# Performance work log

Hardware: AMD Instinct MI355X
Metric: run time of the kernel (lower is better)

## Reference

```python
import jax, jax.numpy as jnp
import numpy as np

B, T, D = 2, 2048, 1024   # batch, seq, d_model
E, K, H = 8, 2, 704       # routed experts, topk, expert hidden
SH = 704 * 2              # shared-expert hidden = moe_hidden * num_shared_experts
EPS = 1e-20               # topk_norm_epsilon
STD = 0.02                # init_weight_std


def setup_inputs() -> dict:
    key = jax.random.key(0)
    ks = jax.random.split(key, 8)
    return {
        "x":   jax.random.normal(ks[0], (B, T, D), jnp.float32),
        "Wg":  jax.random.normal(ks[1], (E, D), jnp.float32) * STD,   # router experts_weights
        "W1":  jax.random.normal(ks[2], (E, D, H), jnp.float32) * STD,  # gate proj per expert
        "W3":  jax.random.normal(ks[3], (E, D, H), jnp.float32) * STD,  # up proj per expert
        "W2":  jax.random.normal(ks[4], (E, H, D), jnp.float32) * STD,  # down proj per expert
        "Ws1": jax.random.normal(ks[5], (D, SH), jnp.float32) * STD,    # shared expert
        "Ws3": jax.random.normal(ks[6], (D, SH), jnp.float32) * STD,
        "Ws2": jax.random.normal(ks[7], (SH, D), jnp.float32) * STD,
    }


def reference(x, Wg, W1, W3, W2, Ws1, Ws3, Ws2):
    b, t, d = x.shape
    n = b * t
    xf = x.reshape(n, d)
    # softmax gating + topk + scatter back into dense [N,E] gate matrix
    gates = jax.nn.softmax(xf @ Wg.T, axis=-1)                      # [N,E]
    top_v, top_i = jax.lax.top_k(gates, K)                          # [N,K]
    masked = jnp.zeros_like(gates).at[jnp.arange(n)[:, None], top_i].set(top_v)
    masked = masked / (masked.sum(-1, keepdims=True) + EPS)         # normalized_moe_gates
    # per-expert SwiGLU FFN over all tokens, then gate-weighted combine
    h = jnp.einsum('nd,edh->enh', xf, W1)                           # [E,N,H]
    g = jnp.einsum('nd,edh->enh', xf, W3)
    y = jnp.einsum('enh,ehd->end', jax.nn.silu(h) * g, W2)          # [E,N,D]
    routed = jnp.einsum('ne,end->nd', masked, y)                    # combine
    shared = (jax.nn.silu(xf @ Ws1) * (xf @ Ws3)) @ Ws2             # shared experts
    return (routed + shared).reshape(b, t, d)
```

## Files before the change

kernel.cpp:

```cpp
#include <hip/hip_runtime.h>
#include <math.h>

typedef __bf16 bf16;
typedef __attribute__((ext_vector_type(8))) __bf16 bf16x8;
typedef __attribute__((ext_vector_type(4))) __bf16 bf16x4;
typedef __attribute__((ext_vector_type(4))) float f32x4;

#define NTOK 4096
#define DM   1024
#define NE   8
#define NEX  10
#define HE   704

#define OFF_CNT   0u
#define OFF_TOK   256u
#define OFF_WGT   131328u
#define OFF_XB    262400u
#define OFF_W1T   8651008u
#define OFF_W3T   20185344u
#define OFF_W2T   31719680u
#define OFF_WS1T  43254016u
#define OFF_WS3T  46137600u
#define OFF_WS2T  49021184u
#define OFF_ACT   51904768u
#define OFF_EIDS  74973440u
#define OFF_GW    74989824u
#define OFF_SLOT  75022592u
#define OFF_YR    OFF_W1T

__device__ __forceinline__ void async_cp16(const bf16* g, bf16* l)
{
    __builtin_amdgcn_global_load_lds(
        (const __attribute__((address_space(1))) unsigned int*)g,
        (__attribute__((address_space(3))) unsigned int*)l, 16, 0, 0);
}

__global__ void cvt_x_kernel(const float* __restrict__ x, bf16* __restrict__ xb, int n4)
{
    int i = blockIdx.x * blockDim.x + threadIdx.x;
    if (i >= n4) return;
    float4 v = ((const float4*)x)[i];
    bf16x4 o;
    o[0] = (bf16)v.x; o[1] = (bf16)v.y; o[2] = (bf16)v.z; o[3] = (bf16)v.w;
    ((bf16x4*)xb)[i] = o;
}

__global__ __launch_bounds__(256) void transpose_all(
    const float* __restrict__ W1, const float* __restrict__ W3, const float* __restrict__ W2,
    const float* __restrict__ Ws1, const float* __restrict__ Ws3, const float* __restrict__ Ws2,
    bf16* __restrict__ w1t, bf16* __restrict__ w3t, bf16* __restrict__ w2t,
    bf16* __restrict__ ws1t, bf16* __restrict__ ws3t, bf16* __restrict__ ws2t)
{
    int id = blockIdx.x;
    const float* src; bf16* dst; int C, rt, ct, nkt;
    if (id < 5632)       { int t = id;         int e = t / 704, m = t % 704; C = 704;
                           src = W1 + (size_t)e * 1024 * 704;  dst = w1t + (size_t)e * 720896;
                           ct = m % 22; rt = m / 22; nkt = 32; }
    else if (id < 11264) { int t = id - 5632;  int e = t / 704, m = t % 704; C = 704;
                           src = W3 + (size_t)e * 1024 * 704;  dst = w3t + (size_t)e * 720896;
                           ct = m % 22; rt = m / 22; nkt = 32; }
    else if (id < 16896) { int t = id - 11264; int e = t / 704, m = t % 704; C = 1024;
                           src = W2 + (size_t)e * 704 * 1024;  dst = w2t + (size_t)e * 720896;
                           ct = m % 32; rt = m / 32; nkt = 22; }
    else if (id < 18304) { int t = id - 16896; C = 1408; src = Ws1;
                           ct = t % 44; rt = t / 44; nkt = 32;
                           int ep = (ct >= 22) ? 1 : 0; ct -= 22 * ep;
                           src += (size_t)704 * ep;
                           dst = ws1t + (size_t)ep * 720896; }
    else if (id < 19712) { int t = id - 18304; C = 1408; src = Ws3;
                           ct = t % 44; rt = t / 44; nkt = 32;
                           int ep = (ct >= 22) ? 1 : 0; ct -= 22 * ep;
                           src += (size_t)704 * ep;
                           dst = ws3t + (size_t)ep * 720896; }
    else                 { int t = id - 19712; C = 1024; src = Ws2;
                           ct = t % 32; rt = t / 32; nkt = 22;
                           int ep = (rt >= 22) ? 1 : 0; rt -= 22 * ep;
                           src += (size_t)704 * 1024 * ep;
                           dst = ws2t + (size_t)ep * 720896; }

    __shared__ float tl[32][33];
    int c0 = ct * 32, r0 = rt * 32;
    int row  = threadIdx.x >> 3;
    int col4 = (threadIdx.x & 7) * 4;
    float4 v = *(const float4*)&src[(size_t)(r0 + row) * C + c0 + col4];
    tl[row][col4 + 0] = v.x; tl[row][col4 + 1] = v.y;
    tl[row][col4 + 2] = v.z; tl[row][col4 + 3] = v.w;
    __syncthreads();
    int n  = c0 + row;
    int ng = n >> 4, nr = n & 15;
    int kt = rt;
    int cc = col4 >> 3, j = col4 & 7;
    bf16x4 o;
    o[0] = (bf16)tl[col4 + 0][row];
    o[1] = (bf16)tl[col4 + 1][row];
    o[2] = (bf16)tl[col4 + 2][row];
    o[3] = (bf16)tl[col4 + 3][row];
    *(bf16x4*)&dst[(size_t)(((ng * nkt + kt) << 9) + (((cc << 4) | nr) << 3) + j)] = o;
}

__global__ __launch_bounds__(256) void router_logits(
    const float* __restrict__ x, const float* __restrict__ Wg,
    int* __restrict__ eids, float2* __restrict__ gw)
{
    int n    = blockIdx.x * 4 + (threadIdx.x >> 6);
    int lane = threadIdx.x & 63;
    const float* xrow = x + (size_t)n * DM;
    float xr[16];
    #pragma unroll
    for (int j = 0; j < 16; j++) xr[j] = xrow[lane + 64 * j];
    float logit[NE];
    #pragma unroll
    for (int e = 0; e < NE; e++) {
        const float* wr = Wg + e * DM;
        float s = 0.f;
        #pragma unroll
        for (int j = 0; j < 16; j++) s += xr[j] * wr[lane + 64 * j];
        #pragma unroll
        for (int off = 32; off; off >>= 1) s += __shfl_xor(s, off, 64);
        logit[e] = s;
    }
    if (lane == 0) {
        int i0 = 0;
        #pragma unroll
        for (int e = 1; e < NE; e++) if (logit[e] > logit[i0]) i0 = e;
        int i1 = (i0 == 0) ? 1 : 0;
        #pragma unroll
        for (int e = 0; e < NE; e++) if (e != i0 && logit[e] > logit[i1]) i1 = e;
        float m = logit[0];
        #pragma unroll
        for (int e = 1; e < NE; e++) m = fmaxf(m, logit[e]);
        float denom = 0.f;
        #pragma unroll
        for (int e = 0; e < NE; e++) denom += expf(logit[e] - m);
        float g0 = expf(logit[i0] - m) / denom;
        float g1 = expf(logit[i1] - m) / denom;
        float inv = 1.f / (g0 + g1 + 1e-20f);
        eids[n] = i0 | (i1 << 16);
        gw[n] = make_float2(g0 * inv, g1 * inv);
    }
}

__global__ __launch_bounds__(128) void build_lists(
    const int* __restrict__ eids, const float2* __restrict__ gw,
    int* __restrict__ cnt, int* __restrict__ tok, float* __restrict__ wgt,
    int2* __restrict__ slots)
{
    __shared__ int lcnt[NE];
    __shared__ int gbase[NE];
    int t = threadIdx.x;
    int n = blockIdx.x * 128 + t;
    if (t < NE) lcnt[t] = 0;
    __syncthreads();
    int packed = eids[n];
    float2 w = gw[n];
    int e0 = packed & 0xffff, e1 = packed >> 16;
    int s0 = atomicAdd(&lcnt[e0], 1);
    int s1 = atomicAdd(&lcnt[e1], 1);
    __syncthreads();
    if (t < NE) gbase[t] = atomicAdd(&cnt[t], lcnt[t]);
    __syncthreads();
    int p0 = gbase[e0] + s0, p1 = gbase[e1] + s1;
    tok[e0 * NTOK + p0] = n; wgt[e0 * NTOK + p0] = w.x;
    tok[e1 * NTOK + p1] = n; wgt[e1 * NTOK + p1] = w.y;
    slots[n] = make_int2((e0 << 16) | p0, (e1 << 16) | p1);
}

__global__ void prefix_kernel(const int* __restrict__ cnt, int* __restrict__ pfx)
{
    if (threadIdx.x == 0) {
        int s = 0;
        for (int e = 0; e < NEX; e++) { pfx[e] = s; s += (e < NE) ? cnt[e] : NTOK; }
        pfx[NEX] = s;
    }
}


__global__ __launch_bounds__(256) void gemm1_swiglu(
    const bf16* __restrict__ xb,
    const bf16* __restrict__ w1t, const bf16* __restrict__ w3t,
    const bf16* __restrict__ ws1t, const bf16* __restrict__ ws3t,
    bf16* __restrict__ act,
    const int* __restrict__ cnt, const int* __restrict__ pfx, const int* __restrict__ tok)
{
    int e = blockIdx.z;
    int count = (e < NE) ? cnt[e] : NTOK;
    int m0 = blockIdx.y * 128;
    if (m0 >= count) return;
    int h0 = blockIdx.x * 64;
    int base = pfx[e];
    const bf16 *B1, *B3;
    if (e < NE) { B1 = w1t + (size_t)e * 720896;        B3 = w3t + (size_t)e * 720896; }
    else        { B1 = ws1t + (size_t)(e - NE) * 720896; B3 = ws3t + (size_t)(e - NE) * 720896; }
    const int* tlist = (e < NE) ? tok + e * NTOK : nullptr;

    __shared__ bf16 As[8 * 512];
    __shared__ bf16 B1s[4 * 512];
    __shared__ bf16 B3s[4 * 512];

    int tid = threadIdx.x, w = tid >> 6, lane = tid & 63;

    int r3 = lane >> 2;
    int cx = (lane & 3) ^ ((r3 >> 1) & 3);
    int sA0 = m0 + 32 * w + r3, sA1 = sA0 + 16;
    int rA0 = tlist ? (sA0 < count ? tlist[sA0] : 0) : (sA0 < count ? sA0 : 0);
    int rA1 = tlist ? (sA1 < count ? tlist[sA1] : 0) : (sA1 < count ? sA1 : 0);
    const bf16* ga0 = xb + (size_t)rA0 * DM + cx * 8;
    const bf16* ga1 = xb + (size_t)rA1 * DM + cx * 8;
    bf16* lA0 = As + (2 * w) * 512;
    bf16* lA1 = As + (2 * w + 1) * 512;
    const bf16* gb1 = B1 + ((size_t)((h0 >> 4) + w) * 32) * 512 + lane * 8;
    const bf16* gb3 = B3 + ((size_t)((h0 >> 4) + w) * 32) * 512 + lane * 8;
    bf16* lB1 = B1s + w * 512;
    bf16* lB3 = B3s + w * 512;

    int rl = lane & 15, ch = lane >> 4;
    int uA = 4 * rl + (ch ^ ((rl >> 1) & 3));
    int gA = (w & 1) * 4;
    int gB = (w >> 1) * 2;
    int wm = (w & 1) * 64, wn = (w >> 1) * 32;

    f32x4 acch[4][2], accg[4][2];
    #pragma unroll
    for (int i = 0; i < 4; i++)
        #pragma unroll
        for (int j = 0; j < 2; j++) {
            acch[i][j] = (f32x4){0.f, 0.f, 0.f, 0.f};
            accg[i][j] = (f32x4){0.f, 0.f, 0.f, 0.f};
        }

    for (int k0 = 0; k0 < DM; k0 += 32) {
        async_cp16(ga0, lA0);
        async_cp16(ga1, lA1);
        async_cp16(gb1, lB1);
        async_cp16(gb3, lB3);
        ga0 += 32; ga1 += 32; gb1 += 512; gb3 += 512;
        __syncthreads();
        bf16x8 af[4], b1f[2], b3f[2];
        #pragma unroll
        for (int i = 0; i < 4; i++) af[i] = *(const bf16x8*)(As + (gA + i) * 512 + uA * 8);
        #pragma unroll
        for (int j = 0; j < 2; j++) {
            b1f[j] = *(const bf16x8*)(B1s + (gB + j) * 512 + lane * 8);
            b3f[j] = *(const bf16x8*)(B3s + (gB + j) * 512 + lane * 8);
        }
        #pragma unroll
        for (int i = 0; i < 4; i++)
            #pragma unroll
            for (int j = 0; j < 2; j++) {
                acch[i][j] = __builtin_amdgcn_mfma_f32_16x16x32_bf16(af[i], b1f[j], acch[i][j], 0, 0, 0);
                accg[i][j] = __builtin_amdgcn_mfma_f32_16x16x32_bf16(af[i], b3f[j], accg[i][j], 0, 0, 0);
            }
        __syncthreads();
    }

    #pragma unroll
    for (int i = 0; i < 4; i++)
        #pragma unroll
        for (int j = 0; j < 2; j++)
            #pragma unroll
            for (int r = 0; r < 4; r++) {
                int row = wm + i * 16 + ch * 4 + r;
                int s2 = m0 + row;
                if (s2 < count) {
                    float hv = acch[i][j][r], gv = accg[i][j][r];
                    float a = hv / (1.f + expf(-hv)) * gv;
                    act[(size_t)(base + s2) * HE + h0 + wn + j * 16 + rl] = (bf16)a;
                }
            }
}

__global__ __launch_bounds__(256) void gemm2_routed(
    const bf16* __restrict__ act,
    const bf16* __restrict__ w2t,
    bf16* __restrict__ yr,
    const int* __restrict__ cnt, const int* __restrict__ pfx,
    const float* __restrict__ wgt)
{
    int e = blockIdx.z;
    int count = cnt[e];
    int m0 = blockIdx.y * 128;
    if (m0 >= count) return;
    int d0 = blockIdx.x * 128;
    int base = pfx[e];
    const bf16* B = w2t + (size_t)e * 720896;
    const float* wl = wgt + e * NTOK;

    __shared__ bf16 As[8 * 512];
    __shared__ bf16 Bs[8 * 512];

    int tid = threadIdx.x, w = tid >> 6, lane = tid & 63;

    int r3 = lane >> 2;
    int cx = (lane & 3) ^ ((r3 >> 1) & 3);
    int sA0 = m0 + 32 * w + r3, sA1 = sA0 + 16;
    int a0 = (sA0 < count) ? (base + sA0) : base;
    int a1 = (sA1 < count) ? (base + sA1) : base;
    const bf16* ga0 = act + (size_t)a0 * HE + cx * 8;
    const bf16* ga1 = act + (size_t)a1 * HE + cx * 8;
    bf16* lA0 = As + (2 * w) * 512;
    bf16* lA1 = As + (2 * w + 1) * 512;
    const bf16* gb0 = B + ((size_t)((d0 >> 4) + 2 * w) * 22) * 512 + lane * 8;
    const bf16* gb1 = B + ((size_t)((d0 >> 4) + 2 * w + 1) * 22) * 512 + lane * 8;
    bf16* lB0 = Bs + (2 * w) * 512;
    bf16* lB1 = Bs + (2 * w + 1) * 512;

    int rl = lane & 15, ch = lane >> 4;
    int uA = 4 * rl + (ch ^ ((rl >> 1) & 3));
    int gA = (w & 1) * 4, gB = (w >> 1) * 4;
    int wm = (w & 1) * 64, wn = (w >> 1) * 64;

    f32x4 acc[4][4];
    #pragma unroll
    for (int i = 0; i < 4; i++)
        #pragma unroll
        for (int j = 0; j < 4; j++) acc[i][j] = (f32x4){0.f, 0.f, 0.f, 0.f};

    for (int kt = 0; kt < 22; kt++) {
        async_cp16(ga0, lA0);
        async_cp16(ga1, lA1);
        async_cp16(gb0, lB0);
        async_cp16(gb1, lB1);
        ga0 += 32; ga1 += 32; gb0 += 512; gb1 += 512;
        __syncthreads();
        bf16x8 af[4], bf_[4];
        #pragma unroll
        for (int i = 0; i < 4; i++) af[i]  = *(const bf16x8*)(As + (gA + i) * 512 + uA * 8);
        #pragma unroll
        for (int j = 0; j < 4; j++) bf_[j] = *(const bf16x8*)(Bs + (gB + j) * 512 + lane * 8);
        #pragma unroll
        for (int i = 0; i < 4; i++)
            #pragma unroll
            for (int j = 0; j < 4; j++)
                acc[i][j] = __builtin_amdgcn_mfma_f32_16x16x32_bf16(af[i], bf_[j], acc[i][j], 0, 0, 0);
        __syncthreads();
    }

    #pragma unroll
    for (int i = 0; i < 4; i++) {
        #pragma unroll
        for (int r = 0; r < 4; r++) {
            int row = wm + i * 16 + ch * 4 + r;
            int s2 = m0 + row;
            if (s2 < count) {
                float wt = wl[s2];
                bf16* yrow = yr + (size_t)(base + s2) * DM + d0 + wn;
                #pragma unroll
                for (int j = 0; j < 4; j++)
                    yrow[j * 16 + rl] = (bf16)(wt * acc[i][j][r]);
            }
        }
    }
}

__global__ __launch_bounds__(256) void gemm2_shared(
    const bf16* __restrict__ act,
    const bf16* __restrict__ ws2t,
    float* __restrict__ out)
{
    int m0 = blockIdx.y * 128;
    int d0 = blockIdx.x * 128;

    __shared__ bf16 As[8 * 512];
    __shared__ bf16 Bs[8 * 512];

    int tid = threadIdx.x, w = tid >> 6, lane = tid & 63;

    int r3 = lane >> 2;
    int cx = (lane & 3) ^ ((r3 >> 1) & 3);
    int sA0 = m0 + 32 * w + r3, sA1 = sA0 + 16;
    bf16* lA0 = As + (2 * w) * 512;
    bf16* lA1 = As + (2 * w + 1) * 512;
    bf16* lB0 = Bs + (2 * w) * 512;
    bf16* lB1 = Bs + (2 * w + 1) * 512;

    int rl = lane & 15, ch = lane >> 4;
    int uA = 4 * rl + (ch ^ ((rl >> 1) & 3));
    int gA = (w & 1) * 4, gB = (w >> 1) * 4;
    int wm = (w & 1) * 64, wn = (w >> 1) * 64;

    f32x4 acc[4][4];
    #pragma unroll
    for (int i = 0; i < 4; i++)
        #pragma unroll
        for (int j = 0; j < 4; j++) acc[i][j] = (f32x4){0.f, 0.f, 0.f, 0.f};

    #pragma unroll
    for (int h = 0; h < 2; h++) {
        int rowbase = 8192 + 4096 * h;
        const bf16* ga0 = act + (size_t)(rowbase + sA0) * HE + cx * 8;
        const bf16* ga1 = act + (size_t)(rowbase + sA1) * HE + cx * 8;
        const bf16* B = ws2t + (size_t)h * 720896;
        const bf16* gb0 = B + ((size_t)((d0 >> 4) + 2 * w) * 22) * 512 + lane * 8;
        const bf16* gb1 = B + ((size_t)((d0 >> 4) + 2 * w + 1) * 22) * 512 + lane * 8;
        for (int kt = 0; kt < 22; kt++) {
            async_cp16(ga0, lA0);
            async_cp16(ga1, lA1);
            async_cp16(gb0, lB0);
            async_cp16(gb1, lB1);
            ga0 += 32; ga1 += 32; gb0 += 512; gb1 += 512;
            __syncthreads();
            bf16x8 af[4], bf_[4];
            #pragma unroll
            for (int i = 0; i < 4; i++) af[i]  = *(const bf16x8*)(As + (gA + i) * 512 + uA * 8);
            #pragma unroll
            for (int j = 0; j < 4; j++) bf_[j] = *(const bf16x8*)(Bs + (gB + j) * 512 + lane * 8);
            #pragma unroll
            for (int i = 0; i < 4; i++)
                #pragma unroll
                for (int j = 0; j < 4; j++)
                    acc[i][j] = __builtin_amdgcn_mfma_f32_16x16x32_bf16(af[i], bf_[j], acc[i][j], 0, 0, 0);
            __syncthreads();
        }
    }

    #pragma unroll
    for (int i = 0; i < 4; i++)
        #pragma unroll
        for (int r = 0; r < 4; r++) {
            int row = wm + i * 16 + ch * 4 + r;
            float* orow = out + (size_t)(m0 + row) * DM + d0 + wn;
            #pragma unroll
            for (int j = 0; j < 4; j++)
                orow[j * 16 + rl] = acc[i][j][r];
        }
}

__global__ __launch_bounds__(256) void fuse_add(
    const bf16* __restrict__ yr, const int2* __restrict__ slots,
    const int* __restrict__ pfx, float* __restrict__ out)
{
    int n = blockIdx.x;
    int2 s = slots[n];
    int slot0 = pfx[s.x >> 16] + (s.x & 0xffff);
    int slot1 = pfx[s.y >> 16] + (s.y & 0xffff);
    const bf16* y0 = yr + (size_t)slot0 * DM;
    const bf16* y1 = yr + (size_t)slot1 * DM;
    float* orow = out + (size_t)n * DM;
    int d = threadIdx.x * 4;
    bf16x4 a = *(const bf16x4*)(y0 + d);
    bf16x4 b = *(const bf16x4*)(y1 + d);
    float4 o = *(float4*)(orow + d);
    o.x += (float)a[0] + (float)b[0];
    o.y += (float)a[1] + (float)b[1];
    o.z += (float)a[2] + (float)b[2];
    o.w += (float)a[3] + (float)b[3];
    *(float4*)(orow + d) = o;
}

extern "C" void kernel_launch(void* const* d_in, const int* in_sizes, int n_in,
                              void* d_out, int out_size, void* d_ws, size_t ws_size,
                              hipStream_t stream)
{
    const float* x   = (const float*)d_in[0];
    const float* Wg  = (const float*)d_in[1];
    const float* W1  = (const float*)d_in[2];
    const float* W3  = (const float*)d_in[3];
    const float* W2  = (const float*)d_in[4];
    const float* Ws1 = (const float*)d_in[5];
    const float* Ws3 = (const float*)d_in[6];
    const float* Ws2 = (const float*)d_in[7];
    float* out = (float*)d_out;
    char*  ws  = (char*)d_ws;

    int*    cnt   = (int*)(ws + OFF_CNT);
    int*    pfx   = (int*)(ws + OFF_CNT + 32);
    int*    tok   = (int*)(ws + OFF_TOK);
    float*  wgt   = (float*)(ws + OFF_WGT);
    bf16*   xb    = (bf16*)(ws + OFF_XB);
    bf16*   w1t   = (bf16*)(ws + OFF_W1T);
    bf16*   w3t   = (bf16*)(ws + OFF_W3T);
    bf16*   w2t   = (bf16*)(ws + OFF_W2T);
    bf16*   ws1t  = (bf16*)(ws + OFF_WS1T);
    bf16*   ws3t  = (bf16*)(ws + OFF_WS3T);
    bf16*   ws2t  = (bf16*)(ws + OFF_WS2T);
    bf16*   act   = (bf16*)(ws + OFF_ACT);
    int*    eids  = (int*)(ws + OFF_EIDS);
    float2* gw    = (float2*)(ws + OFF_GW);
    int2*   slots = (int2*)(ws + OFF_SLOT);
    bf16*   yr    = (bf16*)(ws + OFF_YR);

    hipMemsetAsync(ws, 0, 256, stream);

    cvt_x_kernel<<<4096, 256, 0, stream>>>(x, xb, NTOK * DM / 4);
    transpose_all<<<21120, 256, 0, stream>>>(W1, W3, W2, Ws1, Ws3, Ws2,
                                             w1t, w3t, w2t, ws1t, ws3t, ws2t);
    router_logits<<<1024, 256, 0, stream>>>(x, Wg, eids, gw);
    build_lists<<<32, 128, 0, stream>>>(eids, gw, cnt, tok, wgt, slots);
    prefix_kernel<<<1, 64, 0, stream>>>(cnt, pfx);

    gemm1_swiglu<<<dim3(HE / 64, 32, NEX), 256, 0, stream>>>(
        xb, w1t, w3t, ws1t, ws3t, act, cnt, pfx, tok);

    gemm2_routed<<<dim3(DM / 128, 32, NE), 256, 0, stream>>>(
        act, w2t, yr, cnt, pfx, wgt);
    gemm2_shared<<<dim3(DM / 128, NTOK / 128, 1), 256, 0, stream>>>(
        act, ws2t, out);
    fuse_add<<<NTOK, 256, 0, stream>>>(yr, slots, pfx, out);
}
```

Before: 321.5 us.

## Compact tile maps, double-buffer GEMM LDS, merge routed and shared down-proj

```diff
diff --git a/kernel.cpp b/kernel.cpp
--- a/kernel.cpp
+++ b/kernel.cpp
@@ -24,6 +24,8 @@
 #define OFF_WS2T  49021184u
 #define OFF_ACT   51904768u
 #define OFF_EIDS  74973440u
+#define OFF_MAP1  OFF_EIDS
+#define OFF_MAP2  (OFF_EIDS + 2048u)
 #define OFF_GW    74989824u
 #define OFF_SLOT  75022592u
 #define OFF_YR    OFF_W1T
@@ -165,13 +167,28 @@
     slots[n] = make_int2((e0 << 16) | p0, (e1 << 16) | p1);
 }
 
-__global__ void prefix_kernel(const int* __restrict__ cnt, int* __restrict__ pfx)
-{
-    if (threadIdx.x == 0) {
-        int s = 0;
-        for (int e = 0; e < NEX; e++) { pfx[e] = s; s += (e < NE) ? cnt[e] : NTOK; }
-        pfx[NEX] = s;
-    }
+__global__ void prefix_kernel(const int* __restrict__ cnt, int* __restrict__ pfx,
+                              int* __restrict__ map1, int* __restrict__ map2)
+{
+    if (threadIdx.x != 0) return;
+    int s = 0;
+    for (int e = 0; e < NEX; e++) { pfx[e] = s; s += (e < NE) ? cnt[e] : NTOK; }
+    pfx[NEX] = s;
+    int n1 = 0;
+    for (int e = 0; e < NEX; e++) {
+        int c = (e < NE) ? cnt[e] : NTOK;
+        int ntl = (c + 127) >> 7;
+        for (int t = 0; t < ntl; t++) map1[n1++] = (e << 16) | t;
+    }
+    pfx[11] = n1;
+    int n2 = 0;
+    for (int e = 0; e < NE; e++) {
+        int c = cnt[e];
+        int ntl = (c + 127) >> 7;
+        for (int t = 0; t < ntl; t++) map2[n2++] = (e << 16) | t;
+    }
+    for (int t = 0; t < NTOK / 128; t++) map2[n2++] = (NE << 16) | t;
+    pfx[12] = n2;
 }
 
 
@@ -180,22 +197,24 @@
     const bf16* __restrict__ w1t, const bf16* __restrict__ w3t,
     const bf16* __restrict__ ws1t, const bf16* __restrict__ ws3t,
     bf16* __restrict__ act,
-    const int* __restrict__ cnt, const int* __restrict__ pfx, const int* __restrict__ tok)
-{
-    int e = blockIdx.z;
+    const int* __restrict__ cnt, const int* __restrict__ pfx,
+    const int* __restrict__ tok, const int* __restrict__ map)
+{
+    if ((int)blockIdx.y >= pfx[11]) return;
+    int ent = map[blockIdx.y];
+    int e  = ent >> 16;
+    int m0 = (ent & 0xffff) << 7;
     int count = (e < NE) ? cnt[e] : NTOK;
-    int m0 = blockIdx.y * 128;
-    if (m0 >= count) return;
     int h0 = blockIdx.x * 64;
     int base = pfx[e];
     const bf16 *B1, *B3;
-    if (e < NE) { B1 = w1t + (size_t)e * 720896;        B3 = w3t + (size_t)e * 720896; }
+    if (e < NE) { B1 = w1t + (size_t)e * 720896;         B3 = w3t + (size_t)e * 720896; }
     else        { B1 = ws1t + (size_t)(e - NE) * 720896; B3 = ws3t + (size_t)(e - NE) * 720896; }
     const int* tlist = (e < NE) ? tok + e * NTOK : nullptr;
 
-    __shared__ bf16 As[8 * 512];
-    __shared__ bf16 B1s[4 * 512];
-    __shared__ bf16 B3s[4 * 512];
+    __shared__ bf16 As[2][8 * 512];
+    __shared__ bf16 B1s[2][4 * 512];
+    __shared__ bf16 B3s[2][4 * 512];
 
     int tid = threadIdx.x, w = tid >> 6, lane = tid & 63;
 
@@ -206,12 +225,12 @@
     int rA1 = tlist ? (sA1 < count ? tlist[sA1] : 0) : (sA1 < count ? sA1 : 0);
     const bf16* ga0 = xb + (size_t)rA0 * DM + cx * 8;
     const bf16* ga1 = xb + (size_t)rA1 * DM + cx * 8;
-    bf16* lA0 = As + (2 * w) * 512;
-    bf16* lA1 = As + (2 * w + 1) * 512;
     const bf16* gb1 = B1 + ((size_t)((h0 >> 4) + w) * 32) * 512 + lane * 8;
     const bf16* gb3 = B3 + ((size_t)((h0 >> 4) + w) * 32) * 512 + lane * 8;
-    bf16* lB1 = B1s + w * 512;
-    bf16* lB3 = B3s + w * 512;
+    bf16* aA0 = &As[0][0]  + (2 * w) * 512;
+    bf16* aA1 = aA0 + 512;
+    bf16* aB1 = &B1s[0][0] + w * 512;
+    bf16* aB3 = &B3s[0][0] + w * 512;
 
     int rl = lane & 15, ch = lane >> 4;
     int uA = 4 * rl + (ch ^ ((rl >> 1) & 3));
@@ -228,20 +247,29 @@
             accg[i][j] = (f32x4){0.f, 0.f, 0.f, 0.f};
         }
 
-    for (int k0 = 0; k0 < DM; k0 += 32) {
-        async_cp16(ga0, lA0);
-        async_cp16(ga1, lA1);
-        async_cp16(gb1, lB1);
-        async_cp16(gb3, lB3);
-        ga0 += 32; ga1 += 32; gb1 += 512; gb3 += 512;
-        __syncthreads();
+#define STAGE1(buf) do { \
+        async_cp16(ga0, aA0 + (buf) * 4096); \
+        async_cp16(ga1, aA1 + (buf) * 4096); \
+        async_cp16(gb1, aB1 + (buf) * 2048); \
+        async_cp16(gb3, aB3 + (buf) * 2048); \
+        ga0 += 32; ga1 += 32; gb1 += 512; gb3 += 512; \
+    } while (0)
+
+    STAGE1(0);
+    __syncthreads();
+    for (int k0 = 0; k0 < 32; k0++) {
+        int cur = k0 & 1;
+        if (k0 < 31) STAGE1(cur ^ 1);
+        const bf16* Ab  = &As[0][0]  + cur * 4096;
+        const bf16* B1b = &B1s[0][0] + cur * 2048;
+        const bf16* B3b = &B3s[0][0] + cur * 2048;
         bf16x8 af[4], b1f[2], b3f[2];
         #pragma unroll
-        for (int i = 0; i < 4; i++) af[i] = *(const bf16x8*)(As + (gA + i) * 512 + uA * 8);
+        for (int i = 0; i < 4; i++) af[i] = *(const bf16x8*)(Ab + (gA + i) * 512 + uA * 8);
         #pragma unroll
         for (int j = 0; j < 2; j++) {
-            b1f[j] = *(const bf16x8*)(B1s + (gB + j) * 512 + lane * 8);
-            b3f[j] = *(const bf16x8*)(B3s + (gB + j) * 512 + lane * 8);
+            b1f[j] = *(const bf16x8*)(B1b + (gB + j) * 512 + lane * 8);
+            b3f[j] = *(const bf16x8*)(B3b + (gB + j) * 512 + lane * 8);
         }
         #pragma unroll
         for (int i = 0; i < 4; i++)
@@ -252,6 +280,7 @@
             }
         __syncthreads();
     }
+#undef STAGE1
 
     #pragma unroll
     for (int i = 0; i < 4; i++)
@@ -269,45 +298,47 @@
             }
 }
 
-__global__ __launch_bounds__(256) void gemm2_routed(
+__global__ __launch_bounds__(256) void gemm2_all(
     const bf16* __restrict__ act,
-    const bf16* __restrict__ w2t,
-    bf16* __restrict__ yr,
+    const bf16* __restrict__ w2t, const bf16* __restrict__ ws2t,
+    bf16* __restrict__ yr, float* __restrict__ out,
     const int* __restrict__ cnt, const int* __restrict__ pfx,
-    const float* __restrict__ wgt)
-{
-    int e = blockIdx.z;
-    int count = cnt[e];
-    int m0 = blockIdx.y * 128;
-    if (m0 >= count) return;
+    const float* __restrict__ wgt, const int* __restrict__ map)
+{
+    if ((int)blockIdx.y >= pfx[12]) return;
+    int ent = map[blockIdx.y];
+    int e  = ent >> 16;
+    int m0 = (ent & 0xffff) << 7;
     int d0 = blockIdx.x * 128;
-    int base = pfx[e];
-    const bf16* B = w2t + (size_t)e * 720896;
-    const float* wl = wgt + e * NTOK;
-
-    __shared__ bf16 As[8 * 512];
-    __shared__ bf16 Bs[8 * 512];
+
+    __shared__ bf16 As[2][8 * 512];
+    __shared__ bf16 Bs[2][8 * 512];
 
     int tid = threadIdx.x, w = tid >> 6, lane = tid & 63;
 
     int r3 = lane >> 2;
     int cx = (lane & 3) ^ ((r3 >> 1) & 3);
     int sA0 = m0 + 32 * w + r3, sA1 = sA0 + 16;
+    int rl = lane & 15, ch = lane >> 4;
+    int uA = 4 * rl + (ch ^ ((rl >> 1) & 3));
+    int gA = (w & 1) * 4, gB = (w >> 1) * 4;
+    int wm = (w & 1) * 64, wn = (w >> 1) * 64;
+
+    bf16* aA0 = &As[0][0] + (2 * w) * 512;
+    bf16* aA1 = aA0 + 512;
+    bf16* aB0 = &Bs[0][0] + (2 * w) * 512;
+    bf16* aB1 = aB0 + 512;
+
+    int count, base; const bf16* Bp;
+    if (e < NE) { count = cnt[e]; base = pfx[e]; Bp = w2t + (size_t)e * 720896; }
+    else        { count = NTOK;   base = NTOK * 2; Bp = ws2t; }
+
     int a0 = (sA0 < count) ? (base + sA0) : base;
     int a1 = (sA1 < count) ? (base + sA1) : base;
     const bf16* ga0 = act + (size_t)a0 * HE + cx * 8;
     const bf16* ga1 = act + (size_t)a1 * HE + cx * 8;
-    bf16* lA0 = As + (2 * w) * 512;
-    bf16* lA1 = As + (2 * w + 1) * 512;
-    const bf16* gb0 = B + ((size_t)((d0 >> 4) + 2 * w) * 22) * 512 + lane * 8;
-    const bf16* gb1 = B + ((size_t)((d0 >> 4) + 2 * w + 1) * 22) * 512 + lane * 8;
-    bf16* lB0 = Bs + (2 * w) * 512;
-    bf16* lB1 = Bs + (2 * w + 1) * 512;
-
-    int rl = lane & 15, ch = lane >> 4;
-    int uA = 4 * rl + (ch ^ ((rl >> 1) & 3));
-    int gA = (w & 1) * 4, gB = (w >> 1) * 4;
-    int wm = (w & 1) * 64, wn = (w >> 1) * 64;
+    const bf16* gb0 = Bp + ((size_t)((d0 >> 4) + 2 * w) * 22) * 512 + lane * 8;
+    const bf16* gb1 = Bp + ((size_t)((d0 >> 4) + 2 * w + 1) * 22) * 512 + lane * 8;
 
     f32x4 acc[4][4];
     #pragma unroll
@@ -315,18 +346,38 @@
         #pragma unroll
         for (int j = 0; j < 4; j++) acc[i][j] = (f32x4){0.f, 0.f, 0.f, 0.f};
 
-    for (int kt = 0; kt < 22; kt++) {
-        async_cp16(ga0, lA0);
-        async_cp16(ga1, lA1);
-        async_cp16(gb0, lB0);
-        async_cp16(gb1, lB1);
-        ga0 += 32; ga1 += 32; gb0 += 512; gb1 += 512;
-        __syncthreads();
+#define STAGE2(buf) do { \
+        async_cp16(ga0, aA0 + (buf) * 4096); \
+        async_cp16(ga1, aA1 + (buf) * 4096); \
+        async_cp16(gb0, aB0 + (buf) * 4096); \
+        async_cp16(gb1, aB1 + (buf) * 4096); \
+        ga0 += 32; ga1 += 32; gb0 += 512; gb1 += 512; \
+    } while (0)
+
+    int total = (e < NE) ? 22 : 44;
+    STAGE2(0);
+    int ns = 1;
+    __syncthreads();
+    for (int kt = 0; kt < total; kt++) {
+        int cur = kt & 1;
+        if (ns < total) {
+            if (ns == 22) {
+                ga0 = act + (size_t)(12288 + sA0) * HE + cx * 8;
+                ga1 = act + (size_t)(12288 + sA1) * HE + cx * 8;
+                const bf16* B2 = ws2t + 720896;
+                gb0 = B2 + ((size_t)((d0 >> 4) + 2 * w) * 22) * 512 + lane * 8;
+                gb1 = B2 + ((size_t)((d0 >> 4) + 2 * w + 1) * 22) * 512 + lane * 8;
+            }
+            STAGE2(cur ^ 1);
+            ns++;
+        }
+        const bf16* Ab = &As[0][0] + cur * 4096;
+        const bf16* Bb = &Bs[0][0] + cur * 4096;
         bf16x8 af[4], bf_[4];
         #pragma unroll
-        for (int i = 0; i < 4; i++) af[i]  = *(const bf16x8*)(As + (gA + i) * 512 + uA * 8);
-        #pragma unroll
-        for (int j = 0; j < 4; j++) bf_[j] = *(const bf16x8*)(Bs + (gB + j) * 512 + lane * 8);
+        for (int i = 0; i < 4; i++) af[i]  = *(const bf16x8*)(Ab + (gA + i) * 512 + uA * 8);
+        #pragma unroll
+        for (int j = 0; j < 4; j++) bf_[j] = *(const bf16x8*)(Bb + (gB + j) * 512 + lane * 8);
         #pragma unroll
         for (int i = 0; i < 4; i++)
             #pragma unroll
@@ -334,95 +385,38 @@
                 acc[i][j] = __builtin_amdgcn_mfma_f32_16x16x32_bf16(af[i], bf_[j], acc[i][j], 0, 0, 0);
         __syncthreads();
     }
-
-    #pragma unroll
-    for (int i = 0; i < 4; i++) {
-        #pragma unroll
-        for (int r = 0; r < 4; r++) {
-            int row = wm + i * 16 + ch * 4 + r;
-            int s2 = m0 + row;
-            if (s2 < count) {
-                float wt = wl[s2];
-                bf16* yrow = yr + (size_t)(base + s2) * DM + d0 + wn;
+#undef STAGE2
+
+    if (e < NE) {
+        const float* wl = wgt + e * NTOK;
+        #pragma unroll
+        for (int i = 0; i < 4; i++) {
+            #pragma unroll
+            for (int r = 0; r < 4; r++) {
+                int row = wm + i * 16 + ch * 4 + r;
+                int s2 = m0 + row;
+                if (s2 < count) {
+                    float wt = wl[s2];
+                    bf16* yrow = yr + (size_t)(base + s2) * DM + d0 + wn;
+                    #pragma unroll
+                    for (int j = 0; j < 4; j++)
+                        yrow[j * 16 + rl] = (bf16)(wt * acc[i][j][r]);
+                }
+            }
+        }
+    } else {
+        #pragma unroll
+        for (int i = 0; i < 4; i++) {
+            #pragma unroll
+            for (int r = 0; r < 4; r++) {
+                int row = wm + i * 16 + ch * 4 + r;
+                float* orow = out + (size_t)(m0 + row) * DM + d0 + wn;
                 #pragma unroll
                 for (int j = 0; j < 4; j++)
-                    yrow[j * 16 + rl] = (bf16)(wt * acc[i][j][r]);
+                    orow[j * 16 + rl] = acc[i][j][r];
             }
         }
     }
-}
-
-__global__ __launch_bounds__(256) void gemm2_shared(
-    const bf16* __restrict__ act,
-    const bf16* __restrict__ ws2t,
-    float* __restrict__ out)
-{
-    int m0 = blockIdx.y * 128;
-    int d0 = blockIdx.x * 128;
-
-    __shared__ bf16 As[8 * 512];
-    __shared__ bf16 Bs[8 * 512];
-
-    int tid = threadIdx.x, w = tid >> 6, lane = tid & 63;
-
-    int r3 = lane >> 2;
-    int cx = (lane & 3) ^ ((r3 >> 1) & 3);
-    int sA0 = m0 + 32 * w + r3, sA1 = sA0 + 16;
-    bf16* lA0 = As + (2 * w) * 512;
-    bf16* lA1 = As + (2 * w + 1) * 512;
-    bf16* lB0 = Bs + (2 * w) * 512;
-    bf16* lB1 = Bs + (2 * w + 1) * 512;
-
-    int rl = lane & 15, ch = lane >> 4;
-    int uA = 4 * rl + (ch ^ ((rl >> 1) & 3));
-    int gA = (w & 1) * 4, gB = (w >> 1) * 4;
-    int wm = (w & 1) * 64, wn = (w >> 1) * 64;
-
-    f32x4 acc[4][4];
-    #pragma unroll
-    for (int i = 0; i < 4; i++)
-        #pragma unroll
-        for (int j = 0; j < 4; j++) acc[i][j] = (f32x4){0.f, 0.f, 0.f, 0.f};
-
-    #pragma unroll
-    for (int h = 0; h < 2; h++) {
-        int rowbase = 8192 + 4096 * h;
-        const bf16* ga0 = act + (size_t)(rowbase + sA0) * HE + cx * 8;
-        const bf16* ga1 = act + (size_t)(rowbase + sA1) * HE + cx * 8;
-        const bf16* B = ws2t + (size_t)h * 720896;
-        const bf16* gb0 = B + ((size_t)((d0 >> 4) + 2 * w) * 22) * 512 + lane * 8;
-        const bf16* gb1 = B + ((size_t)((d0 >> 4) + 2 * w + 1) * 22) * 512 + lane * 8;
-        for (int kt = 0; kt < 22; kt++) {
-            async_cp16(ga0, lA0);
-            async_cp16(ga1, lA1);
-            async_cp16(gb0, lB0);
-            async_cp16(gb1, lB1);
-            ga0 += 32; ga1 += 32; gb0 += 512; gb1 += 512;
-            __syncthreads();
-            bf16x8 af[4], bf_[4];
-            #pragma unroll
-            for (int i = 0; i < 4; i++) af[i]  = *(const bf16x8*)(As + (gA + i) * 512 + uA * 8);
-            #pragma unroll
-            for (int j = 0; j < 4; j++) bf_[j] = *(const bf16x8*)(Bs + (gB + j) * 512 + lane * 8);
-            #pragma unroll
-            for (int i = 0; i < 4; i++)
-                #pragma unroll
-                for (int j = 0; j < 4; j++)
-                    acc[i][j] = __builtin_amdgcn_mfma_f32_16x16x32_bf16(af[i], bf_[j], acc[i][j], 0, 0, 0);
-            __syncthreads();
-        }
-    }
-
-    #pragma unroll
-    for (int i = 0; i < 4; i++)
-        #pragma unroll
-        for (int r = 0; r < 4; r++) {
-            int row = wm + i * 16 + ch * 4 + r;
-            float* orow = out + (size_t)(m0 + row) * DM + d0 + wn;
-            #pragma unroll
-            for (int j = 0; j < 4; j++)
-                orow[j * 16 + rl] = acc[i][j][r];
-        }
 }
 
 __global__ __launch_bounds__(256) void fuse_add(
@@ -475,6 +469,8 @@
     bf16*   ws2t  = (bf16*)(ws + OFF_WS2T);
     bf16*   act   = (bf16*)(ws + OFF_ACT);
     int*    eids  = (int*)(ws + OFF_EIDS);
+    int*    map1  = (int*)(ws + OFF_MAP1);
+    int*    map2  = (int*)(ws + OFF_MAP2);
     float2* gw    = (float2*)(ws + OFF_GW);
     int2*   slots = (int2*)(ws + OFF_SLOT);
     bf16*   yr    = (bf16*)(ws + OFF_YR);
@@ -486,14 +482,13 @@
                                              w1t, w3t, w2t, ws1t, ws3t, ws2t);
     router_logits<<<1024, 256, 0, stream>>>(x, Wg, eids, gw);
     build_lists<<<32, 128, 0, stream>>>(eids, gw, cnt, tok, wgt, slots);
-    prefix_kernel<<<1, 64, 0, stream>>>(cnt, pfx);
-
-    gemm1_swiglu<<<dim3(HE / 64, 32, NEX), 256, 0, stream>>>(
-        xb, w1t, w3t, ws1t, ws3t, act, cnt, pfx, tok);
-
-    gemm2_routed<<<dim3(DM / 128, 32, NE), 256, 0, stream>>>(
-        act, w2t, yr, cnt, pfx, wgt);
-    gemm2_shared<<<dim3(DM / 128, NTOK / 128, 1), 256, 0, stream>>>(
-        act, ws2t, out);
+    prefix_kernel<<<1, 64, 0, stream>>>(cnt, pfx, map1, map2);
+
+    gemm1_swiglu<<<dim3(HE / 64, 136, 1), 256, 0, stream>>>(
+        xb, w1t, w3t, ws1t, ws3t, act, cnt, pfx, tok, map1);
+
+    gemm2_all<<<dim3(DM / 128, 104, 1), 256, 0, stream>>>(
+        act, w2t, ws2t, yr, out, cnt, pfx, wgt, map2);
+
     fuse_add<<<NTOK, 256, 0, stream>>>(yr, slots, pfx, out);
 }
```

After: 312.7 us. -2.7%, faster.
